# Kernel optimization log

Hardware: AMD Instinct MI355X
Metric: run time of the kernel (lower is better)

Reference implementation:

```python
import jax, jax.numpy as jnp
import numpy as np

NUM_EMB = 1024
EMB_DIM = 256
COMMIT = 0.25
EPS = 1e-12  # matches torch F.normalize eps


def _l2norm(x):
    return x / jnp.maximum(jnp.linalg.norm(x, axis=-1, keepdims=True), EPS)


def setup_inputs() -> dict:
    key = jax.random.key(0)
    k1, k2 = jax.random.split(key)
    inputs = jax.random.normal(k1, (64, 256, 32, 32), dtype=jnp.float32)
    weight = jax.random.uniform(k2, (NUM_EMB, EMB_DIM), dtype=jnp.float32,
                                minval=-1.0 / NUM_EMB, maxval=1.0 / NUM_EMB)
    return {"inputs": inputs, "weight": weight}


def reference(inputs, weight):
    B, D, H, W = inputs.shape
    x = jnp.transpose(inputs, (0, 2, 3, 1))           # [B,H,W,D]
    flat = x.reshape(-1, D)                           # [N,D]
    fn = _l2norm(flat)                                # normalized inputs
    wn = _l2norm(weight)                              # normalized codebook [K,D]
    # squared euclidean distances between unit vectors
    dist = (jnp.sum(fn * fn, axis=1, keepdims=True)
            + jnp.sum(wn * wn, axis=1)
            - 2.0 * fn @ wn.T)                        # [N,K]
    idx = jnp.argmin(dist, axis=1)                    # [N]
    quant = wn[idx].reshape(x.shape)                  # codebook gather == onehot @ wn
    inorm = fn.reshape(x.shape)
    e_loss = jnp.mean((jax.lax.stop_gradient(quant) - inorm) ** 2)
    q_loss = jnp.mean((quant - jax.lax.stop_gradient(inorm)) ** 2)
    loss = q_loss + COMMIT * e_loss
    quant_st = inorm + jax.lax.stop_gradient(quant - inorm)  # straight-through
    return loss, jnp.transpose(quant_st, (0, 3, 1, 2)), idx[:, None]
```

## Files before the change

### kernel.cpp

```cpp
#include <hip/hip_runtime.h>
#include <math.h>

#define NUM_EMB 1024
#define EMB_DIM 256
#define N_ROWS  65536
#define HW      1024
#define QUANT_OFF 1
#define IDX_OFF   (1 + 16777216)
#define LDA 264
#define KSTR 132

typedef unsigned int uint;
typedef _Float16 f16x8 __attribute__((ext_vector_type(8)));
typedef float    f32x4 __attribute__((ext_vector_type(4)));

__device__ __forceinline__ uint umin2(uint a, uint b) { return a < b ? a : b; }
__device__ __forceinline__ uint umax2(uint a, uint b) { return a > b ? a : b; }

__device__ __forceinline__ uint umed3(uint a, uint b, uint c) {
  uint d;
  asm("v_med3_u32 %0, %1, %2, %3" : "=v"(d) : "v"(a), "v"(b), "v"(c));
  return d;
}

__global__ __launch_bounds__(256)
void k_norm_w(const float* __restrict__ w, float* __restrict__ wn,
              _Float16* __restrict__ wh2, double* __restrict__ rinv) {
  const int k = blockIdx.x, t = threadIdx.x;
  const float v = w[(size_t)k * EMB_DIM + t];
  double s = (double)v * (double)v;
  for (int o = 32; o; o >>= 1) s += __shfl_down(s, o);
  __shared__ double ps[4];
  if ((t & 63) == 0) ps[t >> 6] = s;
  __syncthreads();
  const double tot = ps[0] + ps[1] + ps[2] + ps[3];
  const float nv = v / fmaxf((float)sqrt(tot), 1e-12f);
  wn[(size_t)k * EMB_DIM + t] = nv;
  const int chunk = k >> 8, cc = k & 255;
  const int ks = t >> 5, q = (t >> 3) & 3, e = t & 7;
  wh2[(size_t)chunk * 65536 + ks * 8192 + q * 2048 + cc * 8 + e] = (_Float16)nv;
  if (t == 0) rinv[k] = 1.0 / fmax(sqrt(tot), 1e-12);
}

__global__ __launch_bounds__(256, 2)
void k_fused(const float* __restrict__ x, const _Float16* __restrict__ wh2,
             const float* __restrict__ w, const float* __restrict__ wn,
             const double* __restrict__ rinv, float* __restrict__ out) {
  __shared__ __align__(16) _Float16 As[64 * LDA];
  __shared__ uint4 cand_s[64];
  __shared__ int   cw_s[64];
  const int t = threadIdx.x;
  const int blk = blockIdx.x;
  const int b = blk >> 4;
  const int hw0 = (blk & 15) * 64;

  const int lane = t & 63;
  const int q = lane >> 4;
  const int l15 = lane & 15;
  const int w4id = t >> 6;

  const int bvo0 = q * 2048 + (w4id * 64 +  0 + l15) * 8;
  const int bvo1 = q * 2048 + (w4id * 64 + 16 + l15) * 8;
  const int bvo2 = q * 2048 + (w4id * 64 + 32 + l15) * 8;
  const int bvo3 = q * 2048 + (w4id * 64 + 48 + l15) * 8;

#define LOADB(buf, cc, kk)                                            \
  { const _Float16* ksb_ = wh2 + (size_t)((cc) * 8 + (kk)) * 8192;    \
    buf[0] = *(const f16x8*)&ksb_[bvo0];                              \
    buf[1] = *(const f16x8*)&ksb_[bvo1];                              \
    buf[2] = *(const f16x8*)&ksb_[bvo2];                              \
    buf[3] = *(const f16x8*)&ksb_[bvo3]; }

  f16x8 bb[2][4];
  LOADB(bb[0], 0, 0);

  const int r_own = t & 63;
  const int ph = t >> 6;
  float xv[64];
  {
    const float* xb = x + (size_t)b * (EMB_DIM * HW) + hw0 + r_own;
#pragma unroll
    for (int jp = 0; jp < 8; ++jp) {
      const int d0 = ph * 64 + jp * 8;
      f16x8 v;
#pragma unroll
      for (int e = 0; e < 8; ++e) {
        const float f = xb[(size_t)(d0 + e) * HW];
        xv[jp * 8 + e] = f;
        v[e] = (_Float16)f;
      }
      *(f16x8*)&As[r_own * LDA + d0] = v;
    }
  }
  __syncthreads();

  uint t1[16], t2[16];
#pragma unroll
  for (int i = 0; i < 16; ++i) { t1[i] = 0u; t2[i] = 0u; }

#pragma unroll
  for (int c4 = 0; c4 < 4; ++c4) {
    f32x4 acc[4][4];
#pragma unroll
    for (int rt = 0; rt < 4; ++rt)
#pragma unroll
      for (int ct = 0; ct < 4; ++ct) acc[rt][ct] = (f32x4)0.f;

#pragma unroll
    for (int ks = 0; ks < 8; ++ks) {
      const int cb = ks & 1, nb = cb ^ 1;
      if (ks < 7) { LOADB(bb[nb], c4, ks + 1); }
      else if (c4 < 3) { LOADB(bb[nb], c4 + 1, 0); }

      const f16x8 a0 = *(const f16x8*)&As[(0 * 16 + l15) * LDA + ks * 32 + q * 8];
      const f16x8 a1 = *(const f16x8*)&As[(1 * 16 + l15) * LDA + ks * 32 + q * 8];
      const f16x8 a2 = *(const f16x8*)&As[(2 * 16 + l15) * LDA + ks * 32 + q * 8];
      const f16x8 a3 = *(const f16x8*)&As[(3 * 16 + l15) * LDA + ks * 32 + q * 8];

      __builtin_amdgcn_s_setprio(1);
#pragma unroll
      for (int ct = 0; ct < 4; ++ct) {
        acc[0][ct] = __builtin_amdgcn_mfma_f32_16x16x32_f16(a0, bb[cb][ct], acc[0][ct], 0, 0, 0);
        acc[1][ct] = __builtin_amdgcn_mfma_f32_16x16x32_f16(a1, bb[cb][ct], acc[1][ct], 0, 0, 0);
        acc[2][ct] = __builtin_amdgcn_mfma_f32_16x16x32_f16(a2, bb[cb][ct], acc[2][ct], 0, 0, 0);
        acc[3][ct] = __builtin_amdgcn_mfma_f32_16x16x32_f16(a3, bb[cb][ct], acc[3][ct], 0, 0, 0);
      }
      __builtin_amdgcn_s_setprio(0);
    }

#pragma unroll
    for (int ct = 0; ct < 4; ++ct) {
      const uint idxv = (uint)(c4 * 256 + w4id * 64 + ct * 16 + l15);
#pragma unroll
      for (int rt = 0; rt < 4; ++rt)
#pragma unroll
        for (int r = 0; r < 4; ++r) {
          const float v = fmaxf(acc[rt][ct][r], 0.0f);
          const uint key = (__float_as_uint(v) & 0xFFFFFC00u) | idxv;
          const int slot = rt * 4 + r;
          t2[slot] = umed3(key, t1[slot], t2[slot]);
          t1[slot] = umax2(key, t1[slot]);
        }
    }
  }
#undef LOADB

  __syncthreads();
  uint* keys = (uint*)As;
#pragma unroll
  for (int slot = 0; slot < 16; ++slot) {
    const int rt = slot >> 2, r = slot & 3;
    const int row = rt * 16 + q * 4 + r;
    const int col = w4id * 32 + l15 * 2;
    keys[row * KSTR + col] = t1[slot];
    keys[row * KSTR + col + 1] = t2[slot];
  }
  __syncthreads();
  {
    const int row = t >> 2, seg = t & 3;
    uint s1 = 0, s2 = 0;
#pragma unroll
    for (int i = 0; i < 8; ++i) {
      const int ii = (i + t) & 7;
      const uint4 k4 = *(const uint4*)&keys[row * KSTR + seg * 32 + ii * 4];
      const uint kk[4] = {k4.x, k4.y, k4.z, k4.w};
#pragma unroll
      for (int e = 0; e < 4; ++e) {
        s2 = umed3(kk[e], s1, s2);
        s1 = umax2(kk[e], s1);
      }
    }
    __syncthreads();
    keys[t * 2] = s1;
    keys[t * 2 + 1] = s2;
  }
  __syncthreads();
  if (t < 64) {
    uint c0 = 0, c1 = 0, c2 = 0, c3 = 0;
#pragma unroll
    for (int i = 0; i < 8; ++i) {
      const uint k = keys[t * 8 + i];
      const uint n0 = umin2(c0, k); c0 = umax2(c0, k);
      const uint n1 = umin2(c1, n0); c1 = umax2(c1, n0);
      const uint n2 = umin2(c2, n1); c2 = umax2(c2, n1);
      c3 = umax2(c3, n2);
    }
    uint4 o; o.x = c0; o.y = c1; o.z = c2; o.w = c3;
    cand_s[t] = o;
  }
  __syncthreads();

  double* red = (double*)As;
  {
    const uint4 ck = cand_s[r_own];
    const uint cv[4] = {ck.x, ck.y, ck.z, ck.w};
    double sxx_p = 0.0;
#pragma unroll
    for (int i = 0; i < 64; ++i) sxx_p = fma((double)xv[i], (double)xv[i], sxx_p);
#pragma unroll
    for (int j = 0; j < 4; ++j) {
      const int c = (int)(cv[j] & 1023u);
      const float* wr = w + (size_t)c * EMB_DIM + ph * 64;
      double s = 0.0;
#pragma unroll
      for (int k = 0; k < 16; ++k) {
        const float4 wv = *(const float4*)&wr[k * 4];
        s = fma((double)xv[k * 4 + 0], (double)wv.x, s);
        s = fma((double)xv[k * 4 + 1], (double)wv.y, s);
        s = fma((double)xv[k * 4 + 2], (double)wv.z, s);
        s = fma((double)xv[k * 4 + 3], (double)wv.w, s);
      }
      red[t * 5 + j] = s;
    }
    red[t * 5 + 4] = sxx_p;
  }
  __syncthreads();

  if (t < 64) {
    const uint4 ck = cand_s[t];
    const uint cv[4] = {ck.x, ck.y, ck.z, ck.w};
    double sj[4] = {0.0, 0.0, 0.0, 0.0};
    double sxx = 0.0;
#pragma unroll
    for (int p = 0; p < 4; ++p) {
      const int base = (p * 64 + t) * 5;
      sj[0] += red[base + 0];
      sj[1] += red[base + 1];
      sj[2] += red[base + 2];
      sj[3] += red[base + 3];
      sxx   += red[base + 4];
    }
    double qbest = -1e300; int cw = 1 << 30;
#pragma unroll
    for (int j = 0; j < 4; ++j) {
      const int c = (int)(cv[j] & 1023u);
      const double qj = sj[j] * rinv[c];
      if (qj > qbest || (qj == qbest && c < cw)) { qbest = qj; cw = c; }
    }
    const double dmin = 2.0 - 2.0 * qbest / fmax(sqrt(sxx), 1e-12);
    out[IDX_OFF + blk * 64 + t] = (float)cw;
    cw_s[t] = cw;
    double v = dmin;
    v += __shfl_down(v, 32);
    v += __shfl_down(v, 16);
    v += __shfl_down(v, 8);
    v += __shfl_down(v, 4);
    v += __shfl_down(v, 2);
    v += __shfl_down(v, 1);
    if (t == 0)
      atomicAdd(out, (float)(1.25 * v / 16777216.0));
  }
  __syncthreads();

  float* qs = (float*)As;
  const int rw = t >> 3, li = t & 7;
#pragma unroll 1
  for (int half = 0; half < 2; ++half) {
    const int cw = cw_s[half * 32 + rw];
    const float* wr = wn + (size_t)cw * EMB_DIM;
#pragma unroll
    for (int k = 0; k < 8; ++k) {
      const int d0 = k * 32 + li * 4;
      const float4 wv = *(const float4*)&wr[d0];
      qs[(d0 + 0) * 33 + rw] = wv.x;
      qs[(d0 + 1) * 33 + rw] = wv.y;
      qs[(d0 + 2) * 33 + rw] = wv.z;
      qs[(d0 + 3) * 33 + rw] = wv.w;
    }
    __syncthreads();
    {
      const int hw4 = (t & 7) * 4, dbase = t >> 3;
      float* qout = out + QUANT_OFF + (size_t)b * (EMB_DIM * HW) + hw0 + half * 32;
#pragma unroll
      for (int jj = 0; jj < 8; ++jj) {
        const int d = jj * 32 + dbase;
        float4 v4;
        v4.x = qs[d * 33 + hw4 + 0];
        v4.y = qs[d * 33 + hw4 + 1];
        v4.z = qs[d * 33 + hw4 + 2];
        v4.w = qs[d * 33 + hw4 + 3];
        *(float4*)&qout[(size_t)d * HW + hw4] = v4;
      }
    }
    __syncthreads();
  }
}

extern "C" void kernel_launch(void* const* d_in, const int* in_sizes, int n_in,
                              void* d_out, int out_size, void* d_ws, size_t ws_size,
                              hipStream_t stream) {
  const float* x = (const float*)d_in[0];
  const float* w = (const float*)d_in[1];
  float* out = (float*)d_out;

  char* ws = (char*)d_ws;
  float*     wn   = (float*)ws;
  _Float16*  wh2  = (_Float16*)(ws + 1048576);
  double*    rinv = (double*)(ws + 1048576 + 524288);

  hipMemsetAsync(d_out, 0, sizeof(float), stream);
  hipLaunchKernelGGL(k_norm_w, dim3(NUM_EMB), dim3(256), 0, stream, w, wn, wh2, rinv);
  hipLaunchKernelGGL(k_fused, dim3(N_ROWS / 64), dim3(256), 0, stream, x, wh2, w, wn, rinv, out);
}
```

Before: 185.4 us.

## Halve rows per block to raise occupancy, deepen B prefetch, drop LDS transpose

Each block now handles 32 rows instead of 64, doubling the grid and raising launch bounds to 4 blocks per CU. The codebook fragment prefetch becomes a three-deep ring. The fp32 activations are reloaded from global memory for the fp64 rescoring instead of being held in 64 registers. The quantized-output LDS transpose is replaced with direct strided scalar stores. The aim is more occupancy and less register pressure, at the cost of re-reading the codebook per block twice as often, re-reading x, and storing the output with less coalescing.

```diff
diff --git a/kernel.cpp b/kernel.cpp
--- a/kernel.cpp
+++ b/kernel.cpp
@@ -42,17 +42,17 @@
   if (t == 0) rinv[k] = 1.0 / fmax(sqrt(tot), 1e-12);
 }
 
-__global__ __launch_bounds__(256, 2)
+__global__ __launch_bounds__(256, 4)
 void k_fused(const float* __restrict__ x, const _Float16* __restrict__ wh2,
              const float* __restrict__ w, const float* __restrict__ wn,
              const double* __restrict__ rinv, float* __restrict__ out) {
-  __shared__ __align__(16) _Float16 As[64 * LDA];
-  __shared__ uint4 cand_s[64];
-  __shared__ int   cw_s[64];
+  __shared__ __align__(16) _Float16 As[32 * LDA];
+  __shared__ uint4 cand_s[32];
+  __shared__ int   cw_s[32];
   const int t = threadIdx.x;
   const int blk = blockIdx.x;
-  const int b = blk >> 4;
-  const int hw0 = (blk & 15) * 64;
+  const int b = blk >> 5;
+  const int hw0 = (blk & 31) * 32;
 
   const int lane = t & 63;
   const int q = lane >> 4;
@@ -64,66 +64,58 @@
   const int bvo2 = q * 2048 + (w4id * 64 + 32 + l15) * 8;
   const int bvo3 = q * 2048 + (w4id * 64 + 48 + l15) * 8;
 
-#define LOADB(buf, cc, kk)                                            \
-  { const _Float16* ksb_ = wh2 + (size_t)((cc) * 8 + (kk)) * 8192;    \
-    buf[0] = *(const f16x8*)&ksb_[bvo0];                              \
-    buf[1] = *(const f16x8*)&ksb_[bvo1];                              \
-    buf[2] = *(const f16x8*)&ksb_[bvo2];                              \
+#define LOADB(buf, s)                                       \
+  { const _Float16* ksb_ = wh2 + (size_t)(s) * 8192;        \
+    buf[0] = *(const f16x8*)&ksb_[bvo0];                    \
+    buf[1] = *(const f16x8*)&ksb_[bvo1];                    \
+    buf[2] = *(const f16x8*)&ksb_[bvo2];                    \
     buf[3] = *(const f16x8*)&ksb_[bvo3]; }
 
-  f16x8 bb[2][4];
-  LOADB(bb[0], 0, 0);
-
-  const int r_own = t & 63;
-  const int ph = t >> 6;
-  float xv[64];
+  f16x8 bb[3][4];
+  LOADB(bb[0], 0);
+  LOADB(bb[1], 1);
+
+  const int r_own = t & 31;
+  const int ph = t >> 5;
   {
     const float* xb = x + (size_t)b * (EMB_DIM * HW) + hw0 + r_own;
 #pragma unroll
-    for (int jp = 0; jp < 8; ++jp) {
-      const int d0 = ph * 64 + jp * 8;
+    for (int jp = 0; jp < 4; ++jp) {
+      const int d0 = ph * 32 + jp * 8;
       f16x8 v;
 #pragma unroll
-      for (int e = 0; e < 8; ++e) {
-        const float f = xb[(size_t)(d0 + e) * HW];
-        xv[jp * 8 + e] = f;
-        v[e] = (_Float16)f;
-      }
+      for (int e = 0; e < 8; ++e)
+        v[e] = (_Float16)xb[(size_t)(d0 + e) * HW];
       *(f16x8*)&As[r_own * LDA + d0] = v;
     }
   }
   __syncthreads();
 
-  uint t1[16], t2[16];
-#pragma unroll
-  for (int i = 0; i < 16; ++i) { t1[i] = 0u; t2[i] = 0u; }
+  uint t1[8], t2[8];
+#pragma unroll
+  for (int i = 0; i < 8; ++i) { t1[i] = 0u; t2[i] = 0u; }
 
 #pragma unroll
   for (int c4 = 0; c4 < 4; ++c4) {
-    f32x4 acc[4][4];
-#pragma unroll
-    for (int rt = 0; rt < 4; ++rt)
+    f32x4 acc[2][4];
+#pragma unroll
+    for (int rt = 0; rt < 2; ++rt)
 #pragma unroll
       for (int ct = 0; ct < 4; ++ct) acc[rt][ct] = (f32x4)0.f;
 
 #pragma unroll
     for (int ks = 0; ks < 8; ++ks) {
-      const int cb = ks & 1, nb = cb ^ 1;
-      if (ks < 7) { LOADB(bb[nb], c4, ks + 1); }
-      else if (c4 < 3) { LOADB(bb[nb], c4 + 1, 0); }
-
-      const f16x8 a0 = *(const f16x8*)&As[(0 * 16 + l15) * LDA + ks * 32 + q * 8];
-      const f16x8 a1 = *(const f16x8*)&As[(1 * 16 + l15) * LDA + ks * 32 + q * 8];
-      const f16x8 a2 = *(const f16x8*)&As[(2 * 16 + l15) * LDA + ks * 32 + q * 8];
-      const f16x8 a3 = *(const f16x8*)&As[(3 * 16 + l15) * LDA + ks * 32 + q * 8];
+      const int s = c4 * 8 + ks;
+      if (s + 2 < 32) { LOADB(bb[(s + 2) % 3], s + 2); }
+
+      const f16x8 a0 = *(const f16x8*)&As[( 0 + l15) * LDA + ks * 32 + q * 8];
+      const f16x8 a1 = *(const f16x8*)&As[(16 + l15) * LDA + ks * 32 + q * 8];
 
       __builtin_amdgcn_s_setprio(1);
 #pragma unroll
       for (int ct = 0; ct < 4; ++ct) {
-        acc[0][ct] = __builtin_amdgcn_mfma_f32_16x16x32_f16(a0, bb[cb][ct], acc[0][ct], 0, 0, 0);
-        acc[1][ct] = __builtin_amdgcn_mfma_f32_16x16x32_f16(a1, bb[cb][ct], acc[1][ct], 0, 0, 0);
-        acc[2][ct] = __builtin_amdgcn_mfma_f32_16x16x32_f16(a2, bb[cb][ct], acc[2][ct], 0, 0, 0);
-        acc[3][ct] = __builtin_amdgcn_mfma_f32_16x16x32_f16(a3, bb[cb][ct], acc[3][ct], 0, 0, 0);
+        acc[0][ct] = __builtin_amdgcn_mfma_f32_16x16x32_f16(a0, bb[s % 3][ct], acc[0][ct], 0, 0, 0);
+        acc[1][ct] = __builtin_amdgcn_mfma_f32_16x16x32_f16(a1, bb[s % 3][ct], acc[1][ct], 0, 0, 0);
       }
       __builtin_amdgcn_s_setprio(0);
     }
@@ -132,7 +124,7 @@
     for (int ct = 0; ct < 4; ++ct) {
       const uint idxv = (uint)(c4 * 256 + w4id * 64 + ct * 16 + l15);
 #pragma unroll
-      for (int rt = 0; rt < 4; ++rt)
+      for (int rt = 0; rt < 2; ++rt)
 #pragma unroll
         for (int r = 0; r < 4; ++r) {
           const float v = fmaxf(acc[rt][ct][r], 0.0f);
@@ -148,7 +140,7 @@
   __syncthreads();
   uint* keys = (uint*)As;
 #pragma unroll
-  for (int slot = 0; slot < 16; ++slot) {
+  for (int slot = 0; slot < 8; ++slot) {
     const int rt = slot >> 2, r = slot & 3;
     const int row = rt * 16 + q * 4 + r;
     const int col = w4id * 32 + l15 * 2;
@@ -157,12 +149,12 @@
   }
   __syncthreads();
   {
-    const int row = t >> 2, seg = t & 3;
+    const int row = t >> 3, seg = t & 7;
     uint s1 = 0, s2 = 0;
 #pragma unroll
-    for (int i = 0; i < 8; ++i) {
-      const int ii = (i + t) & 7;
-      const uint4 k4 = *(const uint4*)&keys[row * KSTR + seg * 32 + ii * 4];
+    for (int i = 0; i < 4; ++i) {
+      const int ii = (i + t) & 3;
+      const uint4 k4 = *(const uint4*)&keys[row * KSTR + seg * 16 + ii * 4];
       const uint kk[4] = {k4.x, k4.y, k4.z, k4.w};
 #pragma unroll
       for (int e = 0; e < 4; ++e) {
@@ -175,11 +167,11 @@
     keys[t * 2 + 1] = s2;
   }
   __syncthreads();
-  if (t < 64) {
+  if (t < 32) {
     uint c0 = 0, c1 = 0, c2 = 0, c3 = 0;
 #pragma unroll
-    for (int i = 0; i < 8; ++i) {
-      const uint k = keys[t * 8 + i];
+    for (int i = 0; i < 16; ++i) {
+      const uint k = keys[t * 16 + i];
       const uint n0 = umin2(c0, k); c0 = umax2(c0, k);
       const uint n1 = umin2(c1, n0); c1 = umax2(c1, n0);
       const uint n2 = umin2(c2, n1); c2 = umax2(c2, n1);
@@ -194,21 +186,26 @@
   {
     const uint4 ck = cand_s[r_own];
     const uint cv[4] = {ck.x, ck.y, ck.z, ck.w};
+    const float* xr = x + (size_t)b * (EMB_DIM * HW) + hw0 + r_own;
+    float xf[32];
+#pragma unroll
+    for (int i = 0; i < 32; ++i)
+      xf[i] = xr[(size_t)(ph * 32 + i) * HW];
     double sxx_p = 0.0;
 #pragma unroll
-    for (int i = 0; i < 64; ++i) sxx_p = fma((double)xv[i], (double)xv[i], sxx_p);
+    for (int i = 0; i < 32; ++i) sxx_p = fma((double)xf[i], (double)xf[i], sxx_p);
 #pragma unroll
     for (int j = 0; j < 4; ++j) {
       const int c = (int)(cv[j] & 1023u);
-      const float* wr = w + (size_t)c * EMB_DIM + ph * 64;
+      const float* wr = w + (size_t)c * EMB_DIM + ph * 32;
       double s = 0.0;
 #pragma unroll
-      for (int k = 0; k < 16; ++k) {
+      for (int k = 0; k < 8; ++k) {
         const float4 wv = *(const float4*)&wr[k * 4];
-        s = fma((double)xv[k * 4 + 0], (double)wv.x, s);
-        s = fma((double)xv[k * 4 + 1], (double)wv.y, s);
-        s = fma((double)xv[k * 4 + 2], (double)wv.z, s);
-        s = fma((double)xv[k * 4 + 3], (double)wv.w, s);
+        s = fma((double)xf[k * 4 + 0], (double)wv.x, s);
+        s = fma((double)xf[k * 4 + 1], (double)wv.y, s);
+        s = fma((double)xf[k * 4 + 2], (double)wv.z, s);
+        s = fma((double)xf[k * 4 + 3], (double)wv.w, s);
       }
       red[t * 5 + j] = s;
     }
@@ -216,14 +213,14 @@
   }
   __syncthreads();
 
-  if (t < 64) {
+  if (t < 32) {
     const uint4 ck = cand_s[t];
     const uint cv[4] = {ck.x, ck.y, ck.z, ck.w};
     double sj[4] = {0.0, 0.0, 0.0, 0.0};
     double sxx = 0.0;
 #pragma unroll
-    for (int p = 0; p < 4; ++p) {
-      const int base = (p * 64 + t) * 5;
+    for (int p = 0; p < 8; ++p) {
+      const int base = (p * 32 + t) * 5;
       sj[0] += red[base + 0];
       sj[1] += red[base + 1];
       sj[2] += red[base + 2];
@@ -238,10 +235,9 @@
       if (qj > qbest || (qj == qbest && c < cw)) { qbest = qj; cw = c; }
     }
     const double dmin = 2.0 - 2.0 * qbest / fmax(sqrt(sxx), 1e-12);
-    out[IDX_OFF + blk * 64 + t] = (float)cw;
+    out[IDX_OFF + blk * 32 + t] = (float)cw;
     cw_s[t] = cw;
     double v = dmin;
-    v += __shfl_down(v, 32);
     v += __shfl_down(v, 16);
     v += __shfl_down(v, 8);
     v += __shfl_down(v, 4);
@@ -252,37 +248,18 @@
   }
   __syncthreads();
 
-  float* qs = (float*)As;
-  const int rw = t >> 3, li = t & 7;
-#pragma unroll 1
-  for (int half = 0; half < 2; ++half) {
-    const int cw = cw_s[half * 32 + rw];
-    const float* wr = wn + (size_t)cw * EMB_DIM;
+  {
+    const int cw = cw_s[r_own];
+    const float* wr = wn + (size_t)cw * EMB_DIM + ph * 32;
+    float* qo = out + QUANT_OFF + (size_t)b * (EMB_DIM * HW) + hw0 + r_own;
 #pragma unroll
     for (int k = 0; k < 8; ++k) {
-      const int d0 = k * 32 + li * 4;
-      const float4 wv = *(const float4*)&wr[d0];
-      qs[(d0 + 0) * 33 + rw] = wv.x;
-      qs[(d0 + 1) * 33 + rw] = wv.y;
-      qs[(d0 + 2) * 33 + rw] = wv.z;
-      qs[(d0 + 3) * 33 + rw] = wv.w;
-    }
-    __syncthreads();
-    {
-      const int hw4 = (t & 7) * 4, dbase = t >> 3;
-      float* qout = out + QUANT_OFF + (size_t)b * (EMB_DIM * HW) + hw0 + half * 32;
-#pragma unroll
-      for (int jj = 0; jj < 8; ++jj) {
-        const int d = jj * 32 + dbase;
-        float4 v4;
-        v4.x = qs[d * 33 + hw4 + 0];
-        v4.y = qs[d * 33 + hw4 + 1];
-        v4.z = qs[d * 33 + hw4 + 2];
-        v4.w = qs[d * 33 + hw4 + 3];
-        *(float4*)&qout[(size_t)d * HW + hw4] = v4;
-      }
-    }
-    __syncthreads();
+      const float4 wv = *(const float4*)&wr[k * 4];
+      qo[(size_t)(ph * 32 + k * 4 + 0) * HW] = wv.x;
+      qo[(size_t)(ph * 32 + k * 4 + 1) * HW] = wv.y;
+      qo[(size_t)(ph * 32 + k * 4 + 2) * HW] = wv.z;
+      qo[(size_t)(ph * 32 + k * 4 + 3) * HW] = wv.w;
+    }
   }
 }
 
@@ -300,5 +277,5 @@
 
   hipMemsetAsync(d_out, 0, sizeof(float), stream);
   hipLaunchKernelGGL(k_norm_w, dim3(NUM_EMB), dim3(256), 0, stream, w, wn, wh2, rinv);
-  hipLaunchKernelGGL(k_fused, dim3(N_ROWS / 64), dim3(256), 0, stream, x, wh2, w, wn, rinv, out);
-}
+  hipLaunchKernelGGL(k_fused, dim3(N_ROWS / 32), dim3(256), 0, stream, x, wh2, w, wn, rinv, out);
+}
```

Measured after the change: 279.1 us. 1.5x slower.

## Drop register-held input copy, deepen B prefetch, write quant directly

Applied to the files above, without the earlier changes.

The 64-float per-thread copy of the input row is no longer kept in registers across the MFMA loop. It is re-read from global memory (likely L2-resident) for the fp64 rescoring, which cuts register pressure and may allow more waves per CU. The B-operand prefetch grows from double to quad buffering with a two-step lookahead, and the c4 loop is no longer unrolled to keep code size down. The quantized-output write drops the LDS transpose and its syncs in favour of direct strided stores, which are still coalesced across the 64 rows. The cost is extra global reads of x and more live B-buffer registers.

```diff
diff --git a/kernel.cpp b/kernel.cpp
--- a/kernel.cpp
+++ b/kernel.cpp
@@ -64,19 +64,19 @@
   const int bvo2 = q * 2048 + (w4id * 64 + 32 + l15) * 8;
   const int bvo3 = q * 2048 + (w4id * 64 + 48 + l15) * 8;
 
-#define LOADB(buf, cc, kk)                                            \
-  { const _Float16* ksb_ = wh2 + (size_t)((cc) * 8 + (kk)) * 8192;    \
-    buf[0] = *(const f16x8*)&ksb_[bvo0];                              \
-    buf[1] = *(const f16x8*)&ksb_[bvo1];                              \
-    buf[2] = *(const f16x8*)&ksb_[bvo2];                              \
+#define LOADB(buf, s)                                       \
+  { const _Float16* ksb_ = wh2 + (size_t)(s) * 8192;        \
+    buf[0] = *(const f16x8*)&ksb_[bvo0];                    \
+    buf[1] = *(const f16x8*)&ksb_[bvo1];                    \
+    buf[2] = *(const f16x8*)&ksb_[bvo2];                    \
     buf[3] = *(const f16x8*)&ksb_[bvo3]; }
 
-  f16x8 bb[2][4];
-  LOADB(bb[0], 0, 0);
+  f16x8 bA[4], bB[4], bC[4], bD[4];
+  LOADB(bA, 0);
+  LOADB(bB, 1);
 
   const int r_own = t & 63;
   const int ph = t >> 6;
-  float xv[64];
   {
     const float* xb = x + (size_t)b * (EMB_DIM * HW) + hw0 + r_own;
 #pragma unroll
@@ -84,11 +84,8 @@
       const int d0 = ph * 64 + jp * 8;
       f16x8 v;
 #pragma unroll
-      for (int e = 0; e < 8; ++e) {
-        const float f = xb[(size_t)(d0 + e) * HW];
-        xv[jp * 8 + e] = f;
-        v[e] = (_Float16)f;
-      }
+      for (int e = 0; e < 8; ++e)
+        v[e] = (_Float16)xb[(size_t)(d0 + e) * HW];
       *(f16x8*)&As[r_own * LDA + d0] = v;
     }
   }
@@ -98,7 +95,24 @@
 #pragma unroll
   for (int i = 0; i < 16; ++i) { t1[i] = 0u; t2[i] = 0u; }
 
-#pragma unroll
+#define MMSTEP(c4v, ksv, CURB, PREB)                                                   \
+  { const int sp_ = (c4v) * 8 + (ksv) + 2;                                             \
+    if (sp_ < 32) { LOADB(PREB, sp_); }                                                \
+    const f16x8 a0 = *(const f16x8*)&As[( 0 + l15) * LDA + (ksv) * 32 + q * 8];        \
+    const f16x8 a1 = *(const f16x8*)&As[(16 + l15) * LDA + (ksv) * 32 + q * 8];        \
+    const f16x8 a2 = *(const f16x8*)&As[(32 + l15) * LDA + (ksv) * 32 + q * 8];        \
+    const f16x8 a3 = *(const f16x8*)&As[(48 + l15) * LDA + (ksv) * 32 + q * 8];        \
+    __builtin_amdgcn_s_setprio(1);                                                     \
+    _Pragma("unroll")                                                                  \
+    for (int ct = 0; ct < 4; ++ct) {                                                   \
+      acc[0][ct] = __builtin_amdgcn_mfma_f32_16x16x32_f16(a0, CURB[ct], acc[0][ct], 0, 0, 0); \
+      acc[1][ct] = __builtin_amdgcn_mfma_f32_16x16x32_f16(a1, CURB[ct], acc[1][ct], 0, 0, 0); \
+      acc[2][ct] = __builtin_amdgcn_mfma_f32_16x16x32_f16(a2, CURB[ct], acc[2][ct], 0, 0, 0); \
+      acc[3][ct] = __builtin_amdgcn_mfma_f32_16x16x32_f16(a3, CURB[ct], acc[3][ct], 0, 0, 0); \
+    }                                                                                  \
+    __builtin_amdgcn_s_setprio(0); }
+
+#pragma unroll 1
   for (int c4 = 0; c4 < 4; ++c4) {
     f32x4 acc[4][4];
 #pragma unroll
@@ -106,27 +120,14 @@
 #pragma unroll
       for (int ct = 0; ct < 4; ++ct) acc[rt][ct] = (f32x4)0.f;
 
-#pragma unroll
-    for (int ks = 0; ks < 8; ++ks) {
-      const int cb = ks & 1, nb = cb ^ 1;
-      if (ks < 7) { LOADB(bb[nb], c4, ks + 1); }
-      else if (c4 < 3) { LOADB(bb[nb], c4 + 1, 0); }
-
-      const f16x8 a0 = *(const f16x8*)&As[(0 * 16 + l15) * LDA + ks * 32 + q * 8];
-      const f16x8 a1 = *(const f16x8*)&As[(1 * 16 + l15) * LDA + ks * 32 + q * 8];
-      const f16x8 a2 = *(const f16x8*)&As[(2 * 16 + l15) * LDA + ks * 32 + q * 8];
-      const f16x8 a3 = *(const f16x8*)&As[(3 * 16 + l15) * LDA + ks * 32 + q * 8];
-
-      __builtin_amdgcn_s_setprio(1);
-#pragma unroll
-      for (int ct = 0; ct < 4; ++ct) {
-        acc[0][ct] = __builtin_amdgcn_mfma_f32_16x16x32_f16(a0, bb[cb][ct], acc[0][ct], 0, 0, 0);
-        acc[1][ct] = __builtin_amdgcn_mfma_f32_16x16x32_f16(a1, bb[cb][ct], acc[1][ct], 0, 0, 0);
-        acc[2][ct] = __builtin_amdgcn_mfma_f32_16x16x32_f16(a2, bb[cb][ct], acc[2][ct], 0, 0, 0);
-        acc[3][ct] = __builtin_amdgcn_mfma_f32_16x16x32_f16(a3, bb[cb][ct], acc[3][ct], 0, 0, 0);
-      }
-      __builtin_amdgcn_s_setprio(0);
-    }
+    MMSTEP(c4, 0, bA, bC);
+    MMSTEP(c4, 1, bB, bD);
+    MMSTEP(c4, 2, bC, bA);
+    MMSTEP(c4, 3, bD, bB);
+    MMSTEP(c4, 4, bA, bC);
+    MMSTEP(c4, 5, bB, bD);
+    MMSTEP(c4, 6, bC, bA);
+    MMSTEP(c4, 7, bD, bB);
 
 #pragma unroll
     for (int ct = 0; ct < 4; ++ct) {
@@ -143,6 +144,7 @@
         }
     }
   }
+#undef MMSTEP
 #undef LOADB
 
   __syncthreads();
@@ -194,9 +196,14 @@
   {
     const uint4 ck = cand_s[r_own];
     const uint cv[4] = {ck.x, ck.y, ck.z, ck.w};
+    const float* xr = x + (size_t)b * (EMB_DIM * HW) + hw0 + r_own;
+    float xf[64];
+#pragma unroll
+    for (int i = 0; i < 64; ++i)
+      xf[i] = xr[(size_t)(ph * 64 + i) * HW];
     double sxx_p = 0.0;
 #pragma unroll
-    for (int i = 0; i < 64; ++i) sxx_p = fma((double)xv[i], (double)xv[i], sxx_p);
+    for (int i = 0; i < 64; ++i) sxx_p = fma((double)xf[i], (double)xf[i], sxx_p);
 #pragma unroll
     for (int j = 0; j < 4; ++j) {
       const int c = (int)(cv[j] & 1023u);
@@ -205,10 +212,10 @@
 #pragma unroll
       for (int k = 0; k < 16; ++k) {
         const float4 wv = *(const float4*)&wr[k * 4];
-        s = fma((double)xv[k * 4 + 0], (double)wv.x, s);
-        s = fma((double)xv[k * 4 + 1], (double)wv.y, s);
-        s = fma((double)xv[k * 4 + 2], (double)wv.z, s);
-        s = fma((double)xv[k * 4 + 3], (double)wv.w, s);
+        s = fma((double)xf[k * 4 + 0], (double)wv.x, s);
+        s = fma((double)xf[k * 4 + 1], (double)wv.y, s);
+        s = fma((double)xf[k * 4 + 2], (double)wv.z, s);
+        s = fma((double)xf[k * 4 + 3], (double)wv.w, s);
       }
       red[t * 5 + j] = s;
     }
@@ -252,37 +259,18 @@
   }
   __syncthreads();
 
-  float* qs = (float*)As;
-  const int rw = t >> 3, li = t & 7;
-#pragma unroll 1
-  for (int half = 0; half < 2; ++half) {
-    const int cw = cw_s[half * 32 + rw];
-    const float* wr = wn + (size_t)cw * EMB_DIM;
-#pragma unroll
-    for (int k = 0; k < 8; ++k) {
-      const int d0 = k * 32 + li * 4;
-      const float4 wv = *(const float4*)&wr[d0];
-      qs[(d0 + 0) * 33 + rw] = wv.x;
-      qs[(d0 + 1) * 33 + rw] = wv.y;
-      qs[(d0 + 2) * 33 + rw] = wv.z;
-      qs[(d0 + 3) * 33 + rw] = wv.w;
-    }
-    __syncthreads();
-    {
-      const int hw4 = (t & 7) * 4, dbase = t >> 3;
-      float* qout = out + QUANT_OFF + (size_t)b * (EMB_DIM * HW) + hw0 + half * 32;
-#pragma unroll
-      for (int jj = 0; jj < 8; ++jj) {
-        const int d = jj * 32 + dbase;
-        float4 v4;
-        v4.x = qs[d * 33 + hw4 + 0];
-        v4.y = qs[d * 33 + hw4 + 1];
-        v4.z = qs[d * 33 + hw4 + 2];
-        v4.w = qs[d * 33 + hw4 + 3];
-        *(float4*)&qout[(size_t)d * HW + hw4] = v4;
-      }
-    }
-    __syncthreads();
+  {
+    const int cw = cw_s[r_own];
+    const float* wr = wn + (size_t)cw * EMB_DIM + ph * 64;
+    float* qo = out + QUANT_OFF + (size_t)b * (EMB_DIM * HW) + hw0 + r_own;
+#pragma unroll
+    for (int k = 0; k < 16; ++k) {
+      const float4 wv = *(const float4*)&wr[k * 4];
+      qo[(size_t)(ph * 64 + k * 4 + 0) * HW] = wv.x;
+      qo[(size_t)(ph * 64 + k * 4 + 1) * HW] = wv.y;
+      qo[(size_t)(ph * 64 + k * 4 + 2) * HW] = wv.z;
+      qo[(size_t)(ph * 64 + k * 4 + 3) * HW] = wv.w;
+    }
   }
 }
 
```

Measured after the change: 321.4 us. 1.73x slower.
